# Optimization experiments

Hardware: AMD Instinct MI355X
Metric: run time of the kernel (lower is better)

The kernel has to match this reference:

```python
import jax, jax.numpy as jnp
import numpy as np

N_NODES = 100000
N_EDGES = 1600000
D = 64            # embedding_dim
D2 = D * D        # GRUCell hidden/input size


def gru_cell(x, h, w_ih, w_hh, b_ih, b_hh):
    # PyTorch GRUCell math. x, h: [D2]; w_ih, w_hh: [3*D2, D2]; b_*: [3*D2]
    gi = w_ih @ x + b_ih
    gh = w_hh @ h + b_hh
    i_r, i_z, i_n = jnp.split(gi, 3)
    h_r, h_z, h_n = jnp.split(gh, 3)
    r = jax.nn.sigmoid(i_r + h_r)
    z = jax.nn.sigmoid(i_z + h_z)
    n = jnp.tanh(i_n + r * h_n)
    return (1.0 - z) * n + z * h


def gcn_layer(x, w, src, dst, edge_norm):
    # dense transform then degree-normalized gather-scatter aggregation
    h = x @ w                                   # [N, D]
    m = h[src] * edge_norm[:, None]             # [E, D] messages
    return jax.ops.segment_sum(m, dst, num_segments=N_NODES)


def setup_inputs() -> dict:
    key = jax.random.key(0)
    ks = jax.random.split(key, 12)
    s = 0.02  # keep GRU gates in a sane range
    return {
        "node_embeddings": jax.random.normal(ks[0], (N_NODES, D), jnp.float32),
        "gc1_weights": jax.random.normal(ks[1], (D, D), jnp.float32) * s,
        "gc2_weights": jax.random.normal(ks[2], (D, D), jnp.float32) * s,
        "gc1_hist": jax.random.normal(ks[3], (D, D), jnp.float32) * s,
        "gc2_hist": jax.random.normal(ks[4], (D, D), jnp.float32) * s,
        "w_ih": jax.random.normal(ks[5], (3 * D2, D2), jnp.float32) * s,
        "w_hh": jax.random.normal(ks[6], (3 * D2, D2), jnp.float32) * s,
        "b_ih": jax.random.normal(ks[7], (3 * D2,), jnp.float32) * s,
        "b_hh": jax.random.normal(ks[8], (3 * D2,), jnp.float32) * s,
        "src": jax.random.randint(ks[9], (N_EDGES,), 0, N_NODES, jnp.int32),
        "dst": jax.random.randint(ks[10], (N_EDGES,), 0, N_NODES, jnp.int32),
    }


def reference(node_embeddings, gc1_weights, gc2_weights, gc1_hist, gc2_hist,
              w_ih, w_hh, b_ih, b_hh, src, dst):
    # --- weight evolution (GRUCell over flattened GCN weights) ---
    w1 = gru_cell(gc1_hist.reshape(-1), gc1_weights.reshape(-1),
                  w_ih, w_hh, b_ih, b_hh).reshape(D, D)
    w2 = gru_cell(gc2_hist.reshape(-1), gc2_weights.reshape(-1),
                  w_ih, w_hh, b_ih, b_hh).reshape(D, D)

    # --- symmetric degree normalization (in-degree, clamped at 1) ---
    deg = jax.ops.segment_sum(jnp.ones_like(dst, jnp.float32), dst,
                              num_segments=N_NODES)
    norm = jnp.clip(deg, 1.0, None) ** -0.5     # [N]
    edge_norm = norm[src] * norm[dst]           # [E]

    # --- two GCN layers ---
    x = jax.nn.relu(gcn_layer(node_embeddings, w1, src, dst, edge_norm))
    x = gcn_layer(x, w2, src, dst, edge_norm)
    return x
```

## Files before the change

### kernel.cpp

```cpp
#include <hip/hip_runtime.h>

typedef unsigned int uint_t;

#define N_NODES 100000
#define N_EDGES 1600000
#define D 64
#define D2 4096
#define D3 12288

#define NPAD 100352u

#define BSHIFT 9
#define BNODES 512
#define NBUCK 196
#define CHUNK 8192
#define CAP   16384

#define GRU_ROWS 4

#define OFF_GI1   0u
#define OFF_GI2   (OFF_GI1 + D3)
#define OFF_GH1   (OFF_GI2 + D3)
#define OFF_GH2   (OFF_GH1 + D3)
#define OFF_W1    (OFF_GH2 + D3)
#define OFF_W2    (OFF_W1 + D2)
#define OFF_DEG   (OFF_W2 + D2)
#define OFF_NORM  (OFF_DEG + NPAD)
#define OFF_ROWS  (OFF_NORM + NPAD)
#define OFF_BCNT  (OFF_ROWS + NPAD)
#define OFF_BBASE (OFF_BCNT + 256u)
#define OFF_BCUR  (OFF_BBASE + 256u)
#define OFF_CSR   (OFF_BCUR + 256u)
#define OFF_H     (OFF_CSR + 1600000u)
#define OFF_AGG1  (OFF_H + 6400000u)

__device__ __forceinline__ float dot4(float4 a, float4 b, float acc) {
    acc = fmaf(a.x, b.x, acc);
    acc = fmaf(a.y, b.y, acc);
    acc = fmaf(a.z, b.z, acc);
    acc = fmaf(a.w, b.w, acc);
    return acc;
}

__device__ __forceinline__ uint_t bfr(float f) {
    uint_t u = __float_as_uint(f);
    u += 0x7FFFu + ((u >> 16) & 1u);
    return u >> 16;
}

__global__ __launch_bounds__(256) void gru_matvec(
    const float* __restrict__ w_ih, const float* __restrict__ w_hh,
    const float* __restrict__ x1, const float* __restrict__ x2,
    const float* __restrict__ h1, const float* __restrict__ h2,
    float* __restrict__ gi1, float* __restrict__ gi2,
    float* __restrict__ gh1, float* __restrict__ gh2)
{
    __shared__ float red[4][GRU_ROWS * 4];
    const int tid = threadIdx.x;
    const int r0  = blockIdx.x * GRU_ROWS;

    float4 fx1[4], fx2[4], fh1[4], fh2[4];
    {
        const float4* vx1 = (const float4*)x1;
        const float4* vx2 = (const float4*)x2;
        const float4* vh1 = (const float4*)h1;
        const float4* vh2 = (const float4*)h2;
#pragma unroll
        for (int c = 0; c < 4; ++c) {
            const int idx = tid + c * 256;
            fx1[c] = vx1[idx]; fx2[c] = vx2[idx];
            fh1[c] = vh1[idx]; fh2[c] = vh2[idx];
        }
    }

    float p[GRU_ROWS][4];
#pragma unroll
    for (int r = 0; r < GRU_ROWS; ++r)
#pragma unroll
        for (int o = 0; o < 4; ++o) p[r][o] = 0.f;

#pragma unroll
    for (int r = 0; r < GRU_ROWS; ++r) {
        const float4* wi = (const float4*)(w_ih + (size_t)(r0 + r) * D2);
        const float4* wh = (const float4*)(w_hh + (size_t)(r0 + r) * D2);
        float4 a[4], b[4];
#pragma unroll
        for (int c = 0; c < 4; ++c) {
            a[c] = wi[tid + c * 256];
            b[c] = wh[tid + c * 256];
        }
#pragma unroll
        for (int c = 0; c < 4; ++c) {
            p[r][0] = dot4(a[c], fx1[c], p[r][0]);
            p[r][1] = dot4(a[c], fx2[c], p[r][1]);
            p[r][2] = dot4(b[c], fh1[c], p[r][2]);
            p[r][3] = dot4(b[c], fh2[c], p[r][3]);
        }
    }

    const int wave = tid >> 6, lane = tid & 63;
#pragma unroll
    for (int k = 0; k < GRU_ROWS * 4; ++k) {
        float v = p[k >> 2][k & 3];
#pragma unroll
        for (int m = 32; m > 0; m >>= 1) v += __shfl_down(v, m, 64);
        if (lane == 0) red[wave][k] = v;
    }
    __syncthreads();
    if (tid < GRU_ROWS * 4) {
        float s = red[0][tid] + red[1][tid] + red[2][tid] + red[3][tid];
        const int row = r0 + (tid >> 2);
        const int o = tid & 3;
        float* outp = (o == 0) ? gi1 : (o == 1) ? gi2 : (o == 2) ? gh1 : gh2;
        outp[row] = s;
    }
}

__global__ __launch_bounds__(256) void gru_gates(
    const float* __restrict__ gi1, const float* __restrict__ gh1,
    const float* __restrict__ gi2, const float* __restrict__ gh2,
    const float* __restrict__ b_ih, const float* __restrict__ b_hh,
    const float* __restrict__ hw1, const float* __restrict__ hw2,
    float* __restrict__ w1, float* __restrict__ w2)
{
    const int j = blockIdx.x * 256 + threadIdx.x;
    const int layer = blockIdx.y;
    const float* gi = layer ? gi2 : gi1;
    const float* gh = layer ? gh2 : gh1;
    const float* hw = layer ? hw2 : hw1;
    float* wo = layer ? w2 : w1;

    float ir = gi[j]          + b_ih[j];
    float hr = gh[j]          + b_hh[j];
    float iz = gi[j + D2]     + b_ih[j + D2];
    float hz = gh[j + D2]     + b_hh[j + D2];
    float in_ = gi[j + 2*D2]  + b_ih[j + 2*D2];
    float hn = gh[j + 2*D2]   + b_hh[j + 2*D2];

    float r = 1.f / (1.f + expf(-(ir + hr)));
    float z = 1.f / (1.f + expf(-(iz + hz)));
    float n = tanhf(in_ + r * hn);
    wo[j] = (1.f - z) * n + z * hw[j];
}

__global__ __launch_bounds__(256) void deg_hist_kernel(
    const int* __restrict__ dst, int* __restrict__ deg, int* __restrict__ bcnt)
{
    __shared__ int hist[256];
    const int tid = threadIdx.x;
    hist[tid] = 0;
    __syncthreads();
    const int stride = gridDim.x * 256;
    for (int e = blockIdx.x * 256 + tid; e < N_EDGES; e += stride) {
        const int d = dst[e];
        atomicAdd(&deg[d], 1);
        atomicAdd(&hist[d >> BSHIFT], 1);
    }
    __syncthreads();
    if (hist[tid]) atomicAdd(&bcnt[tid], hist[tid]);
}

__global__ __launch_bounds__(256) void bucket_scan_kernel(
    const int* __restrict__ bcnt, int* __restrict__ bbase, int* __restrict__ bcur)
{
    __shared__ int tmp[256];
    const int tid = threadIdx.x;
    const int c = bcnt[tid];
    tmp[tid] = c;
    __syncthreads();
    for (int off = 1; off < 256; off <<= 1) {
        int a = tmp[tid];
        int b = (tid >= off) ? tmp[tid - off] : 0;
        __syncthreads();
        tmp[tid] = a + b;
        __syncthreads();
    }
    const int ex = tmp[tid] - c;
    bbase[tid] = ex;
    bcur[tid]  = ex;
}

__global__ __launch_bounds__(256) void norm_kernel(
    const int* __restrict__ deg, float* __restrict__ norm)
{
    const int n = blockIdx.x * 256 + threadIdx.x;
    if (n < N_NODES) norm[n] = 1.0f / sqrtf(fmaxf((float)deg[n], 1.0f));
}

__global__ __launch_bounds__(256) void partition_kernel(
    const int* __restrict__ src, const int* __restrict__ dst,
    int* __restrict__ bcur, int2* __restrict__ pairs)
{
    __shared__ int hist[256];
    __shared__ int lbase[256];
    __shared__ int gbase[256];
    __shared__ int lcur[256];
    __shared__ int2 stage[CHUNK];
    const int tid = threadIdx.x;
    const int e0  = blockIdx.x * CHUNK;
    const int cnt = min(CHUNK, N_EDGES - e0);

    hist[tid] = 0; lcur[tid] = 0;
    __syncthreads();
    for (int i = tid; i < cnt; i += 256)
        atomicAdd(&hist[dst[e0 + i] >> BSHIFT], 1);
    __syncthreads();
    {
        const int c = hist[tid];
        lbase[tid] = c;
        __syncthreads();
        for (int off = 1; off < 256; off <<= 1) {
            int a = lbase[tid];
            int b = (tid >= off) ? lbase[tid - off] : 0;
            __syncthreads();
            lbase[tid] = a + b;
            __syncthreads();
        }
        const int inc = lbase[tid];
        lbase[tid] = inc - c;
        if (c) gbase[tid] = atomicAdd(&bcur[tid], c);
        __syncthreads();
    }
    for (int i = tid; i < cnt; i += 256) {
        const int s = src[e0 + i], d = dst[e0 + i];
        const int b = d >> BSHIFT;
        const int p = lbase[b] + atomicAdd(&lcur[b], 1);
        stage[p] = make_int2(s, d);
    }
    __syncthreads();
    for (int i = tid; i < cnt; i += 256) {
        const int2 v = stage[i];
        const int b = v.y >> BSHIFT;
        pairs[gbase[b] + (i - lbase[b])] = v;
    }
}

__global__ __launch_bounds__(256) void bucket_csr_kernel(
    const int2* __restrict__ pairs, const int* __restrict__ deg,
    const int* __restrict__ bbase, const int* __restrict__ bcnt,
    int* __restrict__ rowstart, int* __restrict__ csr_src)
{
    __shared__ int lofs[BNODES];
    __shared__ int lcur[BNODES];
    __shared__ int pscan[256];
    __shared__ int stage[CAP];
    const int tid = threadIdx.x;
    const int b   = blockIdx.x;
    const int nodeBase = b << BSHIFT;

    const int n0 = nodeBase + 2 * tid;
    const int d0 = (n0     < N_NODES) ? deg[n0]     : 0;
    const int d1 = (n0 + 1 < N_NODES) ? deg[n0 + 1] : 0;
    pscan[tid] = d0 + d1;
    __syncthreads();
    for (int off = 1; off < 256; off <<= 1) {
        int a = pscan[tid];
        int x = (tid >= off) ? pscan[tid - off] : 0;
        __syncthreads();
        pscan[tid] = a + x;
        __syncthreads();
    }
    const int ex = pscan[tid] - (d0 + d1);
    lofs[2 * tid]     = ex;
    lofs[2 * tid + 1] = ex + d0;
    lcur[2 * tid]     = 0;
    lcur[2 * tid + 1] = 0;

    const int base = bbase[b];
    if (n0     < N_NODES) rowstart[n0]     = base + ex;
    if (n0 + 1 < N_NODES) rowstart[n0 + 1] = base + ex + d0;
    __syncthreads();

    const int cnt = bcnt[b];
    if (cnt <= CAP) {
        for (int i = tid; i < cnt; i += 256) {
            const int2 v = pairs[base + i];
            const int ln = v.y - nodeBase;
            const int p  = lofs[ln] + atomicAdd(&lcur[ln], 1);
            stage[p] = v.x;
        }
        __syncthreads();
        for (int i = tid; i < cnt; i += 256)
            csr_src[base + i] = stage[i];
    } else {
        for (int i = tid; i < cnt; i += 256) {
            const int2 v = pairs[base + i];
            const int ln = v.y - nodeBase;
            const int p  = atomicAdd(&lcur[ln], 1);
            csr_src[base + lofs[ln] + p] = v.x;
        }
    }
}

template <bool RELU>
__global__ __launch_bounds__(256) void transform_kernel(
    const float* __restrict__ xin, const float* __restrict__ w,
    const float* __restrict__ norm, unsigned short* __restrict__ outbf)
{
    __shared__ float sw[D * D];
    const int tid = threadIdx.x;
#pragma unroll
    for (int i = 0; i < 16; ++i) sw[tid + i * 256] = w[tid + i * 256];
    __syncthreads();

    const int node = blockIdx.x * 256 + tid;
    if (node >= N_NODES) return;

    float x[D];
    const float4* p = (const float4*)(xin + (size_t)node * D);
#pragma unroll
    for (int i = 0; i < 16; ++i) {
        float4 u = p[i];
        x[i * 4 + 0] = u.x; x[i * 4 + 1] = u.y;
        x[i * 4 + 2] = u.z; x[i * 4 + 3] = u.w;
    }
    if (RELU) {
#pragma unroll
        for (int k = 0; k < D; ++k) x[k] = fmaxf(x[k], 0.f);
    }

    float acc[D];
#pragma unroll
    for (int j = 0; j < D; ++j) acc[j] = 0.f;
#pragma unroll
    for (int k = 0; k < D; ++k) {
        float a = x[k];
#pragma unroll
        for (int j = 0; j < D; ++j) acc[j] = fmaf(a, sw[k * D + j], acc[j]);
    }

    const float nn = norm[node];
    uint_t pk[32];
#pragma unroll
    for (int j = 0; j < 32; ++j)
        pk[j] = bfr(acc[2 * j] * nn) | (bfr(acc[2 * j + 1] * nn) << 16);

    uint4* po = (uint4*)(outbf + (size_t)node * D);
#pragma unroll
    for (int i = 0; i < 8; ++i)
        po[i] = make_uint4(pk[4 * i], pk[4 * i + 1], pk[4 * i + 2], pk[4 * i + 3]);
}

__global__ __launch_bounds__(256) void aggregate_gather(
    const unsigned short* __restrict__ hbf, const int* __restrict__ csr_src,
    const int* __restrict__ rowstart, const int* __restrict__ degv,
    const float* __restrict__ norm, float* __restrict__ out)
{
    const int node = blockIdx.x * 4 + (threadIdx.x >> 6);
    if (node >= N_NODES) return;
    const int lane = threadIdx.x & 63;
    const int grp  = lane >> 4;
    const int lg   = lane & 15;
    const uint2* hp = (const uint2*)hbf;

    const int beg = rowstart[node];
    const int end = beg + degv[node];

    float4 acc = make_float4(0.f, 0.f, 0.f, 0.f);
    for (int base = beg; base < end; base += 64) {
        int p = base + lane;
        int idx = 0;
        if (p < end) idx = csr_src[p];
        const int nb = min(64, end - base);
        const int iters = (nb + 3) >> 2;
        for (int i = 0; i < iters; i += 8) {
            uint2 raw[8]; bool act[8];
#pragma unroll
            for (int u = 0; u < 8; ++u) {
                const int kk = (i + u) * 4 + grp;
                const int s = __shfl(idx, kk, 64);
                act[u] = (kk < nb);
                if (act[u]) raw[u] = hp[(size_t)s * 16 + lg];
            }
#pragma unroll
            for (int u = 0; u < 8; ++u) {
                if (act[u]) {
                    acc.x += __uint_as_float(raw[u].x << 16);
                    acc.y += __uint_as_float(raw[u].x & 0xFFFF0000u);
                    acc.z += __uint_as_float(raw[u].y << 16);
                    acc.w += __uint_as_float(raw[u].y & 0xFFFF0000u);
                }
            }
        }
    }
#pragma unroll
    for (int off = 32; off >= 16; off >>= 1) {
        acc.x += __shfl_down(acc.x, off, 64);
        acc.y += __shfl_down(acc.y, off, 64);
        acc.z += __shfl_down(acc.z, off, 64);
        acc.w += __shfl_down(acc.w, off, 64);
    }
    if (lane < 16) {
        const float nn = norm[node];
        float4 o = make_float4(acc.x * nn, acc.y * nn, acc.z * nn, acc.w * nn);
        *(float4*)(out + (size_t)node * D + (size_t)lane * 4) = o;
    }
}

extern "C" void kernel_launch(void* const* d_in, const int* in_sizes, int n_in,
                              void* d_out, int out_size, void* d_ws, size_t ws_size,
                              hipStream_t stream)
{
    const float* emb  = (const float*)d_in[0];
    const float* gc1w = (const float*)d_in[1];
    const float* gc2w = (const float*)d_in[2];
    const float* gc1h = (const float*)d_in[3];
    const float* gc2h = (const float*)d_in[4];
    const float* w_ih = (const float*)d_in[5];
    const float* w_hh = (const float*)d_in[6];
    const float* b_ih = (const float*)d_in[7];
    const float* b_hh = (const float*)d_in[8];
    const int* src = (const int*)d_in[9];
    const int* dst = (const int*)d_in[10];

    float* ws = (float*)d_ws;
    float* gi1 = ws + OFF_GI1;
    float* gi2 = ws + OFF_GI2;
    float* gh1 = ws + OFF_GH1;
    float* gh2 = ws + OFF_GH2;
    float* w1  = ws + OFF_W1;
    float* w2  = ws + OFF_W2;
    int*   deg = (int*)(ws + OFF_DEG);
    float* nrm = ws + OFF_NORM;
    int*   rows = (int*)(ws + OFF_ROWS);
    int*   bcnt = (int*)(ws + OFF_BCNT);
    int*   bbase = (int*)(ws + OFF_BBASE);
    int*   bcur = (int*)(ws + OFF_BCUR);
    int*   csr  = (int*)(ws + OFF_CSR);
    unsigned short* hbf = (unsigned short*)(ws + OFF_H);
    int2*  pairs = (int2*)(ws + OFF_H + 3200000u);
    float* agg1 = ws + OFF_AGG1;
    float* out  = (float*)d_out;

    hipMemsetAsync(deg, 0, NPAD * sizeof(int), stream);
    hipMemsetAsync(bcnt, 0, 256 * sizeof(int), stream);

    gru_matvec<<<D3 / GRU_ROWS, 256, 0, stream>>>(w_ih, w_hh, gc1h, gc2h,
                                                  gc1w, gc2w, gi1, gi2, gh1, gh2);
    gru_gates<<<dim3(16, 2), 256, 0, stream>>>(gi1, gh1, gi2, gh2,
                                               b_ih, b_hh, gc1w, gc2w, w1, w2);

    deg_hist_kernel<<<512, 256, 0, stream>>>(dst, deg, bcnt);
    bucket_scan_kernel<<<1, 256, 0, stream>>>(bcnt, bbase, bcur);
    norm_kernel<<<(N_NODES + 255) / 256, 256, 0, stream>>>(deg, nrm);
    partition_kernel<<<NBUCK, 256, 0, stream>>>(src, dst, bcur, pairs);
    bucket_csr_kernel<<<NBUCK, 256, 0, stream>>>(pairs, deg, bbase, bcnt, rows, csr);

    transform_kernel<false><<<(N_NODES + 255) / 256, 256, 0, stream>>>(emb, w1, nrm, hbf);
    aggregate_gather<<<(N_NODES + 3) / 4, 256, 0, stream>>>(hbf, csr, rows, deg, nrm, agg1);

    transform_kernel<true><<<(N_NODES + 255) / 256, 256, 0, stream>>>(agg1, w2, nrm, hbf);
    aggregate_gather<<<(N_NODES + 3) / 4, 256, 0, stream>>>(hbf, csr, rows, deg, nrm, out);
}
```

Baseline: 693.7 us.

## Restructure GRU matvec to one row per wave with vectors staged in LDS

The GRU matvec kernel now assigns one weight row to each wave. Blocks of 512 threads cover 8 rows, and the grid is split so the w_ih and w_hh halves go to separate blocks. Each block stages only the two input vectors it needs into shared memory, which removes the cross-wave LDS reduction and holds fewer vectors in registers. The aim is better occupancy and more memory parallelism on the ~400MB weight stream. The cost is that each block reloads its vectors into LDS and pays a barrier.

```diff
diff --git a/kernel.cpp b/kernel.cpp
--- a/kernel.cpp
+++ b/kernel.cpp
@@ -15,8 +15,6 @@
 #define NBUCK 196
 #define CHUNK 8192
 #define CAP   16384
-
-#define GRU_ROWS 4
 
 #define OFF_GI1   0u
 #define OFF_GI2   (OFF_GI1 + D3)
@@ -48,71 +46,58 @@
     return u >> 16;
 }
 
-__global__ __launch_bounds__(256) void gru_matvec(
+__global__ __launch_bounds__(512) void gru_matvec(
     const float* __restrict__ w_ih, const float* __restrict__ w_hh,
     const float* __restrict__ x1, const float* __restrict__ x2,
     const float* __restrict__ h1, const float* __restrict__ h2,
     float* __restrict__ gi1, float* __restrict__ gi2,
     float* __restrict__ gh1, float* __restrict__ gh2)
 {
-    __shared__ float red[4][GRU_ROWS * 4];
-    const int tid = threadIdx.x;
-    const int r0  = blockIdx.x * GRU_ROWS;
-
-    float4 fx1[4], fx2[4], fh1[4], fh2[4];
+    __shared__ float4 sA[1024], sB[1024];
+    const int tid  = threadIdx.x;
+    const int half = (blockIdx.x >= 1536);
+    const int blk  = blockIdx.x - (half ? 1536 : 0);
+
     {
-        const float4* vx1 = (const float4*)x1;
-        const float4* vx2 = (const float4*)x2;
-        const float4* vh1 = (const float4*)h1;
-        const float4* vh2 = (const float4*)h2;
-#pragma unroll
-        for (int c = 0; c < 4; ++c) {
-            const int idx = tid + c * 256;
-            fx1[c] = vx1[idx]; fx2[c] = vx2[idx];
-            fh1[c] = vh1[idx]; fh2[c] = vh2[idx];
-        }
-    }
-
-    float p[GRU_ROWS][4];
-#pragma unroll
-    for (int r = 0; r < GRU_ROWS; ++r)
-#pragma unroll
-        for (int o = 0; o < 4; ++o) p[r][o] = 0.f;
-
-#pragma unroll
-    for (int r = 0; r < GRU_ROWS; ++r) {
-        const float4* wi = (const float4*)(w_ih + (size_t)(r0 + r) * D2);
-        const float4* wh = (const float4*)(w_hh + (size_t)(r0 + r) * D2);
-        float4 a[4], b[4];
-#pragma unroll
-        for (int c = 0; c < 4; ++c) {
-            a[c] = wi[tid + c * 256];
-            b[c] = wh[tid + c * 256];
-        }
-#pragma unroll
-        for (int c = 0; c < 4; ++c) {
-            p[r][0] = dot4(a[c], fx1[c], p[r][0]);
-            p[r][1] = dot4(a[c], fx2[c], p[r][1]);
-            p[r][2] = dot4(b[c], fh1[c], p[r][2]);
-            p[r][3] = dot4(b[c], fh2[c], p[r][3]);
-        }
-    }
+        const float4* va = (const float4*)(half ? h1 : x1);
+        const float4* vb = (const float4*)(half ? h2 : x2);
+#pragma unroll
+        for (int i = 0; i < 2; ++i) {
+            const int k = tid + i * 512;
+            sA[k] = va[k];
+            sB[k] = vb[k];
+        }
+    }
+    __syncthreads();
 
     const int wave = tid >> 6, lane = tid & 63;
-#pragma unroll
-    for (int k = 0; k < GRU_ROWS * 4; ++k) {
-        float v = p[k >> 2][k & 3];
-#pragma unroll
-        for (int m = 32; m > 0; m >>= 1) v += __shfl_down(v, m, 64);
-        if (lane == 0) red[wave][k] = v;
-    }
-    __syncthreads();
-    if (tid < GRU_ROWS * 4) {
-        float s = red[0][tid] + red[1][tid] + red[2][tid] + red[3][tid];
-        const int row = r0 + (tid >> 2);
-        const int o = tid & 3;
-        float* outp = (o == 0) ? gi1 : (o == 1) ? gi2 : (o == 2) ? gh1 : gh2;
-        outp[row] = s;
+    const int row  = blk * 8 + wave;
+    const float4* wr = (const float4*)((half ? w_hh : w_ih) + (size_t)row * D2);
+
+    float p0 = 0.f, p1 = 0.f;
+#pragma unroll
+    for (int g = 0; g < 4; ++g) {
+        float4 a[4];
+#pragma unroll
+        for (int k = 0; k < 4; ++k)
+            a[k] = wr[lane + (g * 4 + k) * 64];
+#pragma unroll
+        for (int k = 0; k < 4; ++k) {
+            const int idx = lane + (g * 4 + k) * 64;
+            p0 = dot4(a[k], sA[idx], p0);
+            p1 = dot4(a[k], sB[idx], p1);
+        }
+    }
+#pragma unroll
+    for (int m = 32; m > 0; m >>= 1) {
+        p0 += __shfl_down(p0, m, 64);
+        p1 += __shfl_down(p1, m, 64);
+    }
+    if (lane == 0) {
+        float* oA = half ? gh1 : gi1;
+        float* oB = half ? gh2 : gi2;
+        oA[row] = p0;
+        oB[row] = p1;
     }
 }
 
@@ -435,8 +420,8 @@
     hipMemsetAsync(deg, 0, NPAD * sizeof(int), stream);
     hipMemsetAsync(bcnt, 0, 256 * sizeof(int), stream);
 
-    gru_matvec<<<D3 / GRU_ROWS, 256, 0, stream>>>(w_ih, w_hh, gc1h, gc2h,
-                                                  gc1w, gc2w, gi1, gi2, gh1, gh2);
+    gru_matvec<<<3072, 512, 0, stream>>>(w_ih, w_hh, gc1h, gc2h,
+                                         gc1w, gc2w, gi1, gi2, gh1, gh2);
     gru_gates<<<dim3(16, 2), 256, 0, stream>>>(gi1, gh1, gi2, gh2,
                                                b_ih, b_hh, gc1w, gc2w, w1, w2);
 
```

Result: slower. 832.0 us (+19.9%).
